# Kernel tuning notes

Hardware: AMD Instinct MI355X
Metric: run time of the kernel (lower is better)

Reference implementation:

```python
import jax, jax.numpy as jnp
import numpy as np

N = 50000      # num_nodes
E = 500000     # num_edges
D_IN = 128     # in_features
D_OUT = 128    # out_features
D_REL = 128    # nrela_dim
NEG_SLOPE = 0.2   # LeakyReLU alpha
RATIO = 0.5       # float ratio -> simple (non-schedule) branch
LN_EPS = 1e-5


def setup_inputs() -> dict:
    key = jax.random.key(0)
    ks = jax.random.split(key, 8)
    edge_index = jax.random.randint(ks[0], (2, E), 0, N, dtype=jnp.int64)
    x = jax.random.normal(ks[1], (N, D_IN), dtype=jnp.float32)
    edge_type_embed = jax.random.normal(ks[2], (E, D_REL), dtype=jnp.float32)
    # learned params (xavier-ish scale)
    W = jax.random.normal(ks[3], (4, 2 * D_OUT + D_REL, D_OUT), dtype=jnp.float32) * 0.05
    a = jax.random.normal(ks[4], (4, D_OUT, 1), dtype=jnp.float32) * 0.05
    xw = jax.random.normal(ks[5], (D_IN, D_OUT), dtype=jnp.float32) * (1.0 / np.sqrt(D_IN))
    xb = jnp.zeros((D_OUT,), dtype=jnp.float32)
    gamma = jnp.ones((D_OUT,), dtype=jnp.float32)
    beta = jnp.zeros((D_OUT,), dtype=jnp.float32)
    return {"edge_index": edge_index, "x": x, "edge_type_embed": edge_type_embed,
            "W": W, "a": a, "xw": xw, "xb": xb, "gamma": gamma, "beta": beta}


def _segment_softmax(score, seg, num_segments):
    # per-source-node softmax over edges (matches torch_geometric softmax util)
    seg_max = jax.ops.segment_max(score, seg, num_segments=num_segments)
    seg_max = jnp.where(jnp.isfinite(seg_max), seg_max, 0.0)  # empty segments
    e = jnp.exp(score - seg_max[seg])
    denom = jax.ops.segment_sum(e, seg, num_segments=num_segments)
    return e / (denom[seg] + 1e-16)


def _one_iter(edge_index, xc, ete, Wi, ai):
    src, dst = edge_index[0], edge_index[1]
    # [E, 2*D_OUT + D_REL] @ [2*D_OUT+D_REL, D_OUT] -> [E, D_OUT]
    edge_h = jnp.concatenate([xc[src], xc[dst], ete], axis=1) @ Wi
    score = jax.nn.leaky_relu(jnp.squeeze(edge_h @ ai, -1), NEG_SLOPE)  # [E]
    alpha = _segment_softmax(score, src, N)
    k = int(E * RATIO)
    _, idx = jax.lax.top_k(alpha, k)
    mask = jnp.zeros((E,), dtype=bool).at[idx].set(True)
    alpha = jnp.where(mask, alpha, 0.0)
    # scatter-add weighted messages back to source nodes
    return jax.ops.segment_sum(alpha[:, None] * edge_h, src, num_segments=N)


def reference(edge_index, x, edge_type_embed, W, a, xw, xb, gamma, beta):
    xc = x @ xw + xb  # x_linear
    for i in range(4):  # fixed 4 aggregation iterations (float-ratio branch)
        xc = _one_iter(edge_index, xc, edge_type_embed, W[i], a[i])
    xc = jax.nn.elu(xc)  # concat=True
    mu = jnp.mean(xc, axis=-1, keepdims=True)
    var = jnp.var(xc, axis=-1, keepdims=True)
    return (xc - mu) * jax.lax.rsqrt(var + LN_EPS) * gamma + beta
```

## Files before the change

kernel.cpp:

```cpp
#include <hip/hip_runtime.h>
#include <math.h>

#define DOUT 128

typedef unsigned short u16;
typedef __attribute__((ext_vector_type(8))) short bf16x8;
typedef __attribute__((ext_vector_type(4))) float f32x4;

static __device__ __forceinline__ f32x4 mfma16x16x32(bf16x8 a, bf16x8 b, f32x4 c) {
  return __builtin_amdgcn_mfma_f32_16x16x32_bf16(a, b, c, 0, 0, 0);
}

static __device__ __forceinline__ short bf16i(int v) {
  return (short)(__float_as_uint((float)v) >> 16);
}

static __device__ __forceinline__ float wsum64(float v) {
#pragma unroll
  for (int off = 32; off > 0; off >>= 1) v += __shfl_xor(v, off, 64);
  return v;
}
static __device__ __forceinline__ float wmax64(float v) {
#pragma unroll
  for (int off = 32; off > 0; off >>= 1) v = fmaxf(v, __shfl_xor(v, off, 64));
  return v;
}
static __device__ __forceinline__ float rsumg(float v) {
  v += __shfl_xor(v, 16, 64);
  v += __shfl_xor(v, 32, 64);
  return v;
}

static __device__ __forceinline__ void split3(float x, u16& h, u16& m, u16& l) {
  unsigned u = __float_as_uint(x);
  unsigned rh = u + 0x7FFFu + ((u >> 16) & 1u);
  h = (u16)(rh >> 16);
  float hf = __uint_as_float(rh & 0xFFFF0000u);
  float d1 = x - hf;
  unsigned v = __float_as_uint(d1);
  unsigned rm = v + 0x7FFFu + ((v >> 16) & 1u);
  m = (u16)(rm >> 16);
  float mf = __uint_as_float(rm & 0xFFFF0000u);
  float d2 = d1 - mf;
  unsigned w2 = __float_as_uint(d2);
  unsigned rl = w2 + 0x7FFFu + ((w2 >> 16) & 1u);
  l = (u16)(rl >> 16);
}

static __device__ __forceinline__ void split3pk(float x0, float x1,
                                                unsigned& h, unsigned& m, unsigned& l) {
  unsigned hp, mp, lp;
  asm("v_cvt_pk_bf16_f32 %0, %1, %2" : "=v"(hp) : "v"(x0), "v"(x1));
  float d0 = x0 - __uint_as_float(hp << 16);
  float d1 = x1 - __uint_as_float(hp & 0xFFFF0000u);
  asm("v_cvt_pk_bf16_f32 %0, %1, %2" : "=v"(mp) : "v"(d0), "v"(d1));
  float e0 = d0 - __uint_as_float(mp << 16);
  float e1 = d1 - __uint_as_float(mp & 0xFFFF0000u);
  asm("v_cvt_pk_bf16_f32 %0, %1, %2" : "=v"(lp) : "v"(e0), "v"(e1));
  h = hp; m = mp; l = lp;
}
static __device__ __forceinline__ void split34pk(float4 v, uint2& h, uint2& m, uint2& lo) {
  split3pk(v.x, v.y, h.x, m.x, lo.x);
  split3pk(v.z, v.w, h.y, m.y, lo.y);
}

__global__ void zero_detect_kernel(int* __restrict__ degcur, unsigned* __restrict__ hists,
                                   unsigned* __restrict__ rep, int* __restrict__ candcnt4,
                                   int N, const void* __restrict__ ei, int* __restrict__ flag,
                                   int E) {
  int i = blockIdx.x * blockDim.x + threadIdx.x;
  if (i < N) degcur[i] = 0;
  if (i < 4096) hists[i] = 0u;
  if (i < 32768) rep[i] = 0u;
  if (i < 4) candcnt4[i] = 0;
  const int* p = (const int*)ei;
  int lim = (E < 65536) ? E : 65536;
  int any = 0;
  for (int j = i; j < lim; j += gridDim.x * blockDim.x) any |= (p[2 * j + 1] != 0);
  if (__any(any))
    if ((threadIdx.x & 63) == 0 && any) atomicOr(flag, 1);
}

__global__ void cvt_deg_kernel(const void* __restrict__ ei, const int* __restrict__ flag,
                               int* __restrict__ src, int* __restrict__ dst,
                               int* __restrict__ degcur, int E) {
  int i = blockIdx.x * blockDim.x + threadIdx.x;
  if (i >= E) return;
  int s, d;
  if (*flag) { const int* p = (const int*)ei; s = p[i]; d = p[E + i]; }
  else { const long long* p = (const long long*)ei; s = (int)p[i]; d = (int)p[(size_t)E + i]; }
  src[i] = s;
  dst[i] = d;
  atomicAdd(&degcur[s], 1);
}

__global__ void scan_rowptr_kernel(int* __restrict__ degcur, int* __restrict__ rowptr, int N) {
  const int tid = threadIdx.x;
  const int lane = tid & 63, wid = tid >> 6;
  __shared__ int wsumS[16];
  __shared__ int sbase;
  if (tid == 0) sbase = 0;
  __syncthreads();
  for (int base = 0; base < N; base += 1024) {
    int i = base + tid;
    int v = (i < N) ? degcur[i] : 0;
    int x = v;
#pragma unroll
    for (int off = 1; off < 64; off <<= 1) {
      int y = __shfl_up(x, off, 64);
      if (lane >= off) x += y;
    }
    if (lane == 63) wsumS[wid] = x;
    __syncthreads();
    int wbase = 0;
#pragma unroll
    for (int w2 = 0; w2 < 16; ++w2) wbase += (w2 < wid) ? wsumS[w2] : 0;
    int excl = sbase + wbase + x - v;
    if (i < N) { rowptr[i] = excl; degcur[i] = excl; }
    __syncthreads();
    if (tid == 1023) sbase += wbase + x;
    __syncthreads();
  }
  if (tid == 0) rowptr[N] = sbase;
}

__global__ void scatter_kernel(const int* __restrict__ src, int* __restrict__ cursor,
                               int* __restrict__ eids, int E) {
  int e = blockIdx.x * blockDim.x + threadIdx.x;
  if (e >= E) return;
  int p = atomicAdd(&cursor[src[e]], 1);
  eids[p] = e;
}

__global__ void sort_eids_kernel(const int* __restrict__ rowptr, int* __restrict__ eids, int N) {
  int n = blockIdx.x * blockDim.x + threadIdx.x;
  if (n >= N) return;
  int p0 = rowptr[n], p1 = rowptr[n + 1];
  for (int i = p0 + 1; i < p1; ++i) {
    int key = eids[i];
    int j = i - 1;
    while (j >= p0 && eids[j] > key) { eids[j + 1] = eids[j]; --j; }
    eids[j + 1] = key;
  }
}

__global__ void wprep_kernel(const float* __restrict__ W, const float* __restrict__ a,
                             float* __restrict__ wa_all, const float* __restrict__ xw,
                             u16* __restrict__ wtH, u16* __restrict__ wtM,
                             u16* __restrict__ wtL) {
  int blk = blockIdx.x;
  int tid = threadIdx.x;
  if (blk < 4) {
    int it = blk, k = tid;
    const float* row = W + ((size_t)it * 384 + k) * DOUT;
    const float* ai = a + (size_t)it * DOUT;
    float acc = 0.f;
    for (int j = 0; j < DOUT; ++j) acc = fmaf(row[j], ai[j], acc);
    wa_all[it * 384 + k] = acc;
    return;
  }
  __shared__ int muS[32];
  {
    int lw = tid & 63, g = lw >> 4;
    bf16x8 aEnc;
#pragma unroll
    for (int j = 0; j < 8; ++j) aEnc[j] = bf16i(8 * g + j + 1);
    f32x4 z = {0.f, 0.f, 0.f, 0.f};
    for (int t0 = 0; t0 < 32; ++t0) {
      int g0 = t0 >> 3, j0 = t0 & 7;
      bf16x8 bOne;
#pragma unroll
      for (int j = 0; j < 8; ++j)
        bOne[j] = (g == g0 && j == j0) ? (short)0x3F80 : (short)0;
      f32x4 d = mfma16x16x32(aEnc, bOne, z);
      if (tid == t0) muS[t0] = ((int)(d[0] + 0.5f) - 1) & 31;
    }
  }
  __syncthreads();
  int b = blk - 4;
  int set, ks;
  const float* srcp;
  if (b < 4) { set = 0; ks = b; srcp = xw; }
  else { set = 1 + (b - 4) / 12; ks = (b - 4) % 12; srcp = W + (size_t)(set - 1) * 384 * DOUT; }
  size_t base = ((size_t)set * 12 + ks) * 4096;
  for (int i = tid; i < 4096; i += blockDim.x) {
    int col = i >> 5, t = i & 31;
    float x = srcp[(size_t)(ks * 32 + muS[t]) * DOUT + col];
    u16 h, m, l;
    split3(x, h, m, l);
    wtH[base + i] = h;
    wtM[base + i] = m;
    wtL[base + i] = l;
  }
}

__global__ __launch_bounds__(256) void et4_kernel(const float* __restrict__ ete,
                                                  const float* __restrict__ wa_all,
                                                  const int* __restrict__ eids,
                                                  const int* __restrict__ dst,
                                                  int* __restrict__ dstp, int* __restrict__ pos,
                                                  float* __restrict__ et4, int E) {
  __shared__ float4 w3s[4][32];
  int tid = threadIdx.x;
  if (tid < 128) {
    int it = tid >> 5, k4 = tid & 31;
    const float* base = wa_all + it * 384 + 256 + k4 * 4;
    w3s[it][k4] = make_float4(base[0], base[1], base[2], base[3]);
  }
  __syncthreads();
  int p = blockIdx.x * blockDim.x + tid;
  if (p >= E) return;
  int e = eids[p];
  dstp[p] = dst[e];
  pos[e] = p;
  const float4* row = (const float4*)(ete + (size_t)e * DOUT);
  float a0 = 0.f, a1 = 0.f, a2 = 0.f, a3 = 0.f;
#pragma unroll
  for (int k4 = 0; k4 < 32; ++k4) {
    float4 r = row[k4];
    float4 w0 = w3s[0][k4], w1 = w3s[1][k4], w2 = w3s[2][k4], w3v = w3s[3][k4];
    a0 = fmaf(r.x, w0.x, fmaf(r.y, w0.y, fmaf(r.z, w0.z, fmaf(r.w, w0.w, a0))));
    a1 = fmaf(r.x, w1.x, fmaf(r.y, w1.y, fmaf(r.z, w1.z, fmaf(r.w, w1.w, a1))));
    a2 = fmaf(r.x, w2.x, fmaf(r.y, w2.y, fmaf(r.z, w2.z, fmaf(r.w, w2.w, a2))));
    a3 = fmaf(r.x, w3v.x, fmaf(r.y, w3v.y, fmaf(r.z, w3v.z, fmaf(r.w, w3v.w, a3))));
  }
  et4[p] = a0;
  et4[(size_t)E + p] = a1;
  et4[(size_t)2 * E + p] = a2;
  et4[(size_t)3 * E + p] = a3;
}

__global__ __launch_bounds__(256) void softmax_kernel(
    const int* __restrict__ rowptr, const int* __restrict__ dstp,
    const float* __restrict__ pa, const float* __restrict__ qa, const float* __restrict__ et4,
    int it, int E, float* __restrict__ alpha, unsigned* __restrict__ rep0, int N) {
  __shared__ unsigned lh[256];
  int tid = threadIdx.x;
  lh[tid] = 0u;
  __syncthreads();
  const float* etp = et4 + (size_t)it * E;
  int w = (int)(((size_t)blockIdx.x * blockDim.x + tid) >> 6);
  int lane = tid & 63;
  if (w < N) {
    int p0 = rowptr[w], p1 = rowptr[w + 1];
    int deg = p1 - p0;
    if (deg > 0) {
      float pan = pa[w];
      if (deg <= 64) {
        int p = p0 + lane;
        int ok = (p < p1);
        float sv = -3.402823466e38f;
        if (ok) {
          float s = pan + qa[dstp[p]] + etp[p];
          sv = (s >= 0.f) ? s : 0.2f * s;
        }
        float m = wmax64(sv);
        float ee = ok ? expf(sv - m) : 0.f;
        float den = 0.f;
        for (int i = 0; i < deg; ++i) den += __shfl(ee, i, 64);
        den += 1e-16f;
        if (ok) {
          float av = ee / den;
          alpha[p] = av;
          atomicAdd(&lh[__float_as_uint(av) >> 24], 1u);
        }
      } else if (deg <= 256) {
        float sv[4]; int okv[4];
#pragma unroll
        for (int u = 0; u < 4; ++u) {
          int p = p0 + u * 64 + lane;
          if (p < p1) {
            okv[u] = 1;
            float s = pan + qa[dstp[p]] + etp[p];
            sv[u] = (s >= 0.f) ? s : 0.2f * s;
          } else { okv[u] = 0; sv[u] = -3.402823466e38f; }
        }
        float m = fmaxf(fmaxf(sv[0], sv[1]), fmaxf(sv[2], sv[3]));
        m = wmax64(m);
        float ssum = 0.f;
#pragma unroll
        for (int u = 0; u < 4; ++u)
          if (okv[u]) { sv[u] = expf(sv[u] - m); ssum += sv[u]; }
        ssum = wsum64(ssum);
        float den = ssum + 1e-16f;
#pragma unroll
        for (int u = 0; u < 4; ++u)
          if (okv[u]) {
            float av = sv[u] / den;
            alpha[p0 + u * 64 + lane] = av;
            atomicAdd(&lh[__float_as_uint(av) >> 24], 1u);
          }
      } else {
        float m = -3.402823466e38f;
        for (int p = p0 + lane; p < p1; p += 64) {
          float s = pan + qa[dstp[p]] + etp[p];
          s = (s >= 0.f) ? s : 0.2f * s;
          m = fmaxf(m, s);
        }
        m = wmax64(m);
        float ssum = 0.f;
        for (int p = p0 + lane; p < p1; p += 64) {
          float s = pan + qa[dstp[p]] + etp[p];
          s = (s >= 0.f) ? s : 0.2f * s;
          ssum += expf(s - m);
        }
        ssum = wsum64(ssum);
        float den = ssum + 1e-16f;
        for (int p = p0 + lane; p < p1; p += 64) {
          float s = pan + qa[dstp[p]] + etp[p];
          s = (s >= 0.f) ? s : 0.2f * s;
          float av = expf(s - m) / den;
          alpha[p] = av;
          atomicAdd(&lh[__float_as_uint(av) >> 24], 1u);
        }
      }
    }
  }
  __syncthreads();
  if (lh[tid]) atomicAdd(&rep0[(blockIdx.x & 31) * 256 + tid], lh[tid]);
}

__device__ __forceinline__ void scan256_one(const unsigned* __restrict__ hist, unsigned krem_in,
                                            unsigned* lds, unsigned* res,
                                            unsigned& bin, unsigned& krem_out) {
  int t = threadIdx.x;
  lds[t] = hist[t];
  __syncthreads();
  for (int off = 1; off < 256; off <<= 1) {
    unsigned add = (t + off < 256) ? lds[t + off] : 0u;
    __syncthreads();
    lds[t] += add;
    __syncthreads();
  }
  {
    unsigned above = (t == 255) ? 0u : lds[t + 1];
    if (lds[t] >= krem_in && above < krem_in) { res[0] = (unsigned)t; res[1] = krem_in - above; }
  }
  __syncthreads();
  bin = res[0];
  krem_out = res[1];
  __syncthreads();
}

__global__ __launch_bounds__(256) void hist1_kernel(const float* __restrict__ alpha,
                                                    const unsigned* __restrict__ rep0,
                                                    unsigned* __restrict__ hists_it,
                                                    unsigned* __restrict__ scanres,
                                                    unsigned Ktop, int E) {
  __shared__ unsigned lds[256], res2[2], lh[256];
  int t = threadIdx.x;
  unsigned v = 0u;
#pragma unroll
  for (int r = 0; r < 32; ++r) v += rep0[r * 256 + t];
  lds[t] = v;
  __syncthreads();
  for (int off = 1; off < 256; off <<= 1) {
    unsigned add = (t + off < 256) ? lds[t + off] : 0u;
    __syncthreads();
    lds[t] += add;
    __syncthreads();
  }
  {
    unsigned above = (t == 255) ? 0u : lds[t + 1];
    if (lds[t] >= Ktop && above < Ktop) { res2[0] = (unsigned)t; res2[1] = Ktop - above; }
  }
  __syncthreads();
  unsigned bin0 = res2[0];
  if (blockIdx.x == 0 && t == 0) { scanres[0] = bin0; scanres[1] = res2[1]; }
  lh[t] = 0u;
  __syncthreads();
  unsigned* myh = hists_it + 256;
  for (int e = blockIdx.x * blockDim.x + t; e < E; e += gridDim.x * blockDim.x) {
    unsigned b = __float_as_uint(alpha[e]);
    if ((b >> 24) == bin0) atomicAdd(&lh[(b >> 16) & 0xFFu], 1u);
  }
  __syncthreads();
  if (lh[t]) atomicAdd(&myh[t], lh[t]);
}

__global__ __launch_bounds__(256) void hist2_kernel(const float* __restrict__ alpha,
                                                    unsigned* __restrict__ hists_it,
                                                    unsigned* __restrict__ scanres, int E) {
  __shared__ unsigned lds[256], res2[2], lh[256];
  int t = threadIdx.x;
  unsigned pref8 = scanres[0], krem0 = scanres[1];
  unsigned bin1, krem1;
  scan256_one(hists_it + 256, krem0, lds, res2, bin1, krem1);
  unsigned pref16 = (pref8 << 8) | bin1;
  if (blockIdx.x == 0 && t == 0) { scanres[2] = pref16; scanres[3] = krem1; }
  lh[t] = 0u;
  __syncthreads();
  unsigned* myh = hists_it + 512;
  for (int e = blockIdx.x * blockDim.x + t; e < E; e += gridDim.x * blockDim.x) {
    unsigned b = __float_as_uint(alpha[e]);
    if ((b >> 16) == pref16) atomicAdd(&lh[(b >> 8) & 0xFFu], 1u);
  }
  __syncthreads();
  if (lh[t]) atomicAdd(&myh[t], lh[t]);
}

__global__ __launch_bounds__(256) void hist3c_kernel(const float* __restrict__ alpha,
                                                     unsigned* __restrict__ hists_it,
                                                     unsigned* __restrict__ scanres,
                                                     int* __restrict__ candList,
                                                     int* __restrict__ candCnt, int E) {
  __shared__ unsigned lds[256], res2[2], lh[256];
  int t = threadIdx.x;
  unsigned pref16 = scanres[2], krem1 = scanres[3];
  unsigned bin2, krem2;
  scan256_one(hists_it + 512, krem1, lds, res2, bin2, krem2);
  unsigned pref24 = (pref16 << 8) | bin2;
  if (blockIdx.x == 0 && t == 0) { scanres[4] = pref24; scanres[5] = krem2; }
  lh[t] = 0u;
  __syncthreads();
  unsigned* myh = hists_it + 768;
  for (int e = blockIdx.x * blockDim.x + t; e < E; e += gridDim.x * blockDim.x) {
    unsigned b = __float_as_uint(alpha[e]);
    if ((b >> 8) == pref24) {
      atomicAdd(&lh[b & 0xFFu], 1u);
      int p = atomicAdd(candCnt, 1);
      if (p < 4096) candList[p] = e;
    }
  }
  __syncthreads();
  if (lh[t]) atomicAdd(&myh[t], lh[t]);
}

__global__ __launch_bounds__(1024) void resolve24_kernel(
    const float* __restrict__ alpha, float* __restrict__ amask,
    const unsigned* __restrict__ hists_it, const unsigned* __restrict__ scanres,
    const int* __restrict__ candList, const int* __restrict__ candCnt,
    const int* __restrict__ eids, const int* __restrict__ pos,
    int* __restrict__ header, int E) {
  __shared__ unsigned lds[256], res2[2];
  int tid = threadIdx.x;
  unsigned pref24 = scanres[4], krem2 = scanres[5];
  {
    int t = tid;
    if (t < 256) lds[t] = hists_it[768 + t];
    __syncthreads();
    for (int off = 1; off < 256; off <<= 1) {
      unsigned add = 0u;
      if (t < 256 && t + off < 256) add = lds[t + off];
      __syncthreads();
      if (t < 256) lds[t] += add;
      __syncthreads();
    }
    if (t < 256) {
      unsigned above = (t == 255) ? 0u : lds[t + 1];
      if (lds[t] >= krem2 && above < krem2) { res2[0] = (unsigned)t; res2[1] = krem2 - above; }
    }
    __syncthreads();
  }
  unsigned thr = (pref24 << 8) | res2[0];
  int needT = (int)res2[1];
  __syncthreads();
  int cc = *candCnt;
  __shared__ int tiel[4096];
  __shared__ int tiec;
  if (tid == 0) tiec = 0;
  __syncthreads();
  if (cc <= 4096) {
    for (int i = tid; i < cc; i += blockDim.x) {
      int p = candList[i];
      if (__float_as_uint(alpha[p]) == thr) {
        int q = atomicAdd(&tiec, 1);
        tiel[q] = eids[p];
      }
    }
    __syncthreads();
    int ce = tiec;
    int dropc = ce - needT;
    if (dropc <= 0) {
      if (tid == 0) { header[0] = 0; header[1] = (int)thr; header[2] = 0; }
      return;
    }
    if (dropc <= 64) {
      int sortN = 64;
      while (sortN < ce) sortN <<= 1;
      for (int i = tid; i < sortN; i += blockDim.x)
        if (i >= ce) tiel[i] = 0x7fffffff;
      __syncthreads();
      for (int k = 2; k <= sortN; k <<= 1) {
        for (int j = k >> 1; j > 0; j >>= 1) {
          for (int i = tid; i < sortN; i += blockDim.x) {
            int ixj = i ^ j;
            if (ixj > i) {
              int v0 = tiel[i], v1 = tiel[ixj];
              bool up = ((i & k) == 0);
              if ((v0 > v1) == up) { tiel[i] = v1; tiel[ixj] = v0; }
            }
          }
          __syncthreads();
        }
      }
      if (tid == 0) { header[0] = 0; header[1] = (int)thr; header[2] = dropc; }
      for (int i = tid; i < dropc; i += blockDim.x) header[3 + i] = tiel[needT + i];
      return;
    }
  }
  if (tid == 0) { header[0] = 1; }
  __shared__ int wtot[16];
  __shared__ int sbase;
  if (tid == 0) sbase = 0;
  __syncthreads();
  int lane = tid & 63, wid = tid >> 6;
  for (int base = 0; base < E; base += 1024) {
    int e = base + tid;
    float a = 0.f; int f = 0; unsigned b = 0u;
    if (e < E) { a = alpha[pos[e]]; b = __float_as_uint(a); f = (b == thr) ? 1 : 0; }
    int x = f;
#pragma unroll
    for (int off = 1; off < 64; off <<= 1) {
      int y = __shfl_up(x, off, 64);
      if (lane >= off) x += y;
    }
    if (lane == 63) wtot[wid] = x;
    __syncthreads();
    int wbase = 0;
#pragma unroll
    for (int w2 = 0; w2 < 16; ++w2) wbase += (w2 < wid) ? wtot[w2] : 0;
    if (e < E) {
      float outv = 0.f;
      if (b > thr) outv = a;
      else if (f && (sbase + wbase + x - f) < needT) outv = a;
      amask[e] = outv;
    }
    __syncthreads();
    if (tid == 1023) sbase += wbase + x;
    __syncthreads();
  }
}

static __device__ __forceinline__ float edge_w2(float av, const float* __restrict__ amask,
                                                const int* __restrict__ hdr, int flg,
                                                unsigned thr, int dc, int e) {
  if (flg) return amask[e];
  unsigned b = __float_as_uint(av);
  if (b > thr) return av;
  if (b == thr) {
    for (int j = 0; j < dc; ++j)
      if (hdr[3 + j] == e) return 0.f;
    return av;
  }
  return 0.f;
}

__global__ void agg_kernel(const int* __restrict__ rowptr, const int* __restrict__ eids,
                           const int* __restrict__ dstp, const float* __restrict__ alpha,
                           const float* __restrict__ amask, const int* __restrict__ hdr,
                           const float* __restrict__ xc, const float* __restrict__ ete,
                           float* __restrict__ sa, float* __restrict__ vbuf,
                           float* __restrict__ tbuf, int N) {
  int w = (int)(((size_t)blockIdx.x * blockDim.x + threadIdx.x) >> 6);
  int lane = threadIdx.x & 63;
  if (w >= N) return;
  const int flg = hdr[0];
  const unsigned thr = (unsigned)hdr[1];
  const int dc = hdr[2];
  int p0 = rowptr[w], p1 = rowptr[w + 1];
  int deg = p1 - p0;
  const int half = lane >> 5;
  const int l32 = lane & 31;
  const float4* xc4 = (const float4*)xc;
  const float4* et4p = (const float4*)ete;
  float4 acc = make_float4(0.f, 0.f, 0.f, 0.f);
  float s = 0.f;
  if (deg <= 64) {
    int p = p0 + lane;
    int e = -1; float am = 0.f; int dd = 0;
    if (p < p1) { e = eids[p]; am = edge_w2(alpha[p], amask, hdr, flg, thr, dc, e); dd = dstp[p]; }
    for (int i = 0; i < deg; ++i) {
      float a = __shfl(am, i, 64);
      if (a != 0.f) {
        int ei = __shfl(e, i, 64);
        int di = __shfl(dd, i, 64);
        const float4* b = half ? (et4p + (size_t)ei * 32) : (xc4 + (size_t)di * 32);
        float4 r = b[l32];
        acc.x = fmaf(a, r.x, acc.x); acc.y = fmaf(a, r.y, acc.y);
        acc.z = fmaf(a, r.z, acc.z); acc.w = fmaf(a, r.w, acc.w);
        s += a;
      }
    }
  } else {
    for (int p = p0; p < p1; ++p) {
      int e0 = eids[p];
      float a0 = edge_w2(alpha[p], amask, hdr, flg, thr, dc, e0);
      if (a0 != 0.f) {
        int d0 = dstp[p];
        const float4* b0 = half ? (et4p + (size_t)e0 * 32) : (xc4 + (size_t)d0 * 32);
        float4 r = b0[l32];
        acc.x = fmaf(a0, r.x, acc.x); acc.y = fmaf(a0, r.y, acc.y);
        acc.z = fmaf(a0, r.z, acc.z); acc.w = fmaf(a0, r.w, acc.w);
        s += a0;
      }
    }
  }
  if (half == 0) ((float4*)vbuf)[(size_t)w * 32 + l32] = acc;
  else           ((float4*)tbuf)[(size_t)w * 32 + l32] = acc;
  if (lane == 0) sa[w] = s;
}

__global__ __launch_bounds__(256) void gemm_mfma_kernel(
    const float* __restrict__ A0, const float* __restrict__ A1, const float* __restrict__ A2,
    const float* __restrict__ sca, const u16* __restrict__ wtH, const u16* __restrict__ wtM,
    const u16* __restrict__ wtL, const float* __restrict__ bias, float* __restrict__ C,
    int N, int nseg,
    const float* __restrict__ wa_next, float* __restrict__ pa, float* __restrict__ qa,
    const float* __restrict__ gamma, const float* __restrict__ beta,
    float* __restrict__ outp, int epi) {
  __shared__ __align__(16) char smem[61440];
  u16 (*AsH)[40] = (u16(*)[40])(smem);
  u16 (*AsM)[40] = (u16(*)[40])(smem + 10240);
  u16 (*AsL)[40] = (u16(*)[40])(smem + 20480);
  u16 (*BsH)[40] = (u16(*)[40])(smem + 30720);
  u16 (*BsM)[40] = (u16(*)[40])(smem + 40960);
  u16 (*BsL)[40] = (u16(*)[40])(smem + 51200);
  const int tid = threadIdx.x;
  const int m0 = blockIdx.x * 128;
  const int K = DOUT * nseg;
  const int w = tid >> 6, l = tid & 63;
  const int cb = l & 15, g = l >> 4;

  int rowlab[4], collab[4];
  {
    bf16x8 enc, ones;
#pragma unroll
    for (int j = 0; j < 8; ++j) { enc[j] = bf16i(cb + 1); ones[j] = (short)0x3F80; }
    f32x4 z = {0.f, 0.f, 0.f, 0.f};
    f32x4 dR = mfma16x16x32(enc, ones, z);
    f32x4 dC = mfma16x16x32(ones, enc, z);
#pragma unroll
    for (int r = 0; r < 4; ++r) {
      rowlab[r] = ((int)(dR[r] * (1.f / 32.f) + 0.5f) - 1) & 15;
      collab[r] = ((int)(dC[r] * (1.f / 32.f) + 0.5f) - 1) & 15;
    }
  }

  f32x4 acc[2][8];
#pragma unroll
  for (int i = 0; i < 2; ++i)
#pragma unroll
    for (int j = 0; j < 8; ++j) acc[i][j] = (f32x4){0.f, 0.f, 0.f, 0.f};

  const int srow = tid >> 1, shalf = tid & 1;
  const int grow_s = m0 + srow;
  float scv = 1.f;
  if (sca && grow_s < N) scv = sca[grow_s];

  auto loadA = [&](int kc, float4& v0, float4& v1, float4& v2, float4& v3) {
    const int seg = kc >> 7;
    const float* Ap = (seg == 0) ? A0 : (seg == 1) ? A1 : A2;
    v0 = make_float4(0.f, 0.f, 0.f, 0.f); v1 = v0; v2 = v0; v3 = v0;
    if (grow_s < N) {
      const float4* p = (const float4*)(Ap + (size_t)grow_s * DOUT + (kc & 127) + shalf * 16);
      v0 = p[0]; v1 = p[1]; v2 = p[2]; v3 = p[3];
      if (seg == 0 && sca) {
        v0.x *= scv; v0.y *= scv; v0.z *= scv; v0.w *= scv;
        v1.x *= scv; v1.y *= scv; v1.z *= scv; v1.w *= scv;
        v2.x *= scv; v2.y *= scv; v2.z *= scv; v2.w *= scv;
        v3.x *= scv; v3.y *= scv; v3.z *= scv; v3.w *= scv;
      }
    }
  };
  auto loadB = [&](int kc, uint4& h0, uint4& h1, uint4& m0u, uint4& m1u, uint4& l0u,
                   uint4& l1u) {
    size_t sb = (size_t)(kc >> 5) << 12;
    const uint4* gh = (const uint4*)(wtH + sb) + tid * 2;
    const uint4* gm = (const uint4*)(wtM + sb) + tid * 2;
    const uint4* gl = (const uint4*)(wtL + sb) + tid * 2;
    h0 = gh[0]; h1 = gh[1];
    m0u = gm[0]; m1u = gm[1];
    l0u = gl[0]; l1u = gl[1];
  };

  float4 av0, av1, av2, av3, nv0, nv1, nv2, nv3;
  uint4 bh0, bh1, bm0u, bm1u, bl0u, bl1u, nh0, nh1, nm0, nm1, nl0, nl1;
  loadA(0, av0, av1, av2, av3);
  loadB(0, bh0, bh1, bm0u, bm1u, bl0u, bl1u);

  const int nks = K >> 5;
  for (int ks = 0; ks < nks; ++ks) {
    const int kc = ks << 5;
    {
      uint2 h0, m0v, l0, h1, m1v, l1, h2, m2v, l2, h3, m3v, l3;
      split34pk(av0, h0, m0v, l0); split34pk(av1, h1, m1v, l1);
      split34pk(av2, h2, m2v, l2); split34pk(av3, h3, m3v, l3);
      *(uint4*)&AsH[srow][shalf * 16]     = make_uint4(h0.x, h0.y, h1.x, h1.y);
      *(uint4*)&AsH[srow][shalf * 16 + 8] = make_uint4(h2.x, h2.y, h3.x, h3.y);
      *(uint4*)&AsM[srow][shalf * 16]     = make_uint4(m0v.x, m0v.y, m1v.x, m1v.y);
      *(uint4*)&AsM[srow][shalf * 16 + 8] = make_uint4(m2v.x, m2v.y, m3v.x, m3v.y);
      *(uint4*)&AsL[srow][shalf * 16]     = make_uint4(l0.x, l0.y, l1.x, l1.y);
      *(uint4*)&AsL[srow][shalf * 16 + 8] = make_uint4(l2.x, l2.y, l3.x, l3.y);
      *(uint4*)&BsH[srow][shalf * 16]     = bh0;
      *(uint4*)&BsH[srow][shalf * 16 + 8] = bh1;
      *(uint4*)&BsM[srow][shalf * 16]     = bm0u;
      *(uint4*)&BsM[srow][shalf * 16 + 8] = bm1u;
      *(uint4*)&BsL[srow][shalf * 16]     = bl0u;
      *(uint4*)&BsL[srow][shalf * 16 + 8] = bl1u;
    }
    if (ks + 1 < nks) {
      loadA(kc + 32, nv0, nv1, nv2, nv3);
      loadB(kc + 32, nh0, nh1, nm0, nm1, nl0, nl1);
    }
    __syncthreads();
    bf16x8 aH0 = *(const bf16x8*)&AsH[w * 32 + cb][g * 8];
    bf16x8 aH1 = *(const bf16x8*)&AsH[w * 32 + 16 + cb][g * 8];
    bf16x8 aM0 = *(const bf16x8*)&AsM[w * 32 + cb][g * 8];
    bf16x8 aM1 = *(const bf16x8*)&AsM[w * 32 + 16 + cb][g * 8];
    bf16x8 aL0 = *(const bf16x8*)&AsL[w * 32 + cb][g * 8];
    bf16x8 aL1 = *(const bf16x8*)&AsL[w * 32 + 16 + cb][g * 8];
#pragma unroll
    for (int ct = 0; ct < 8; ++ct) {
      bf16x8 bH = *(const bf16x8*)&BsH[ct * 16 + cb][g * 8];
      bf16x8 bM = *(const bf16x8*)&BsM[ct * 16 + cb][g * 8];
      bf16x8 bL = *(const bf16x8*)&BsL[ct * 16 + cb][g * 8];
      acc[0][ct] = mfma16x16x32(aH0, bH, acc[0][ct]);
      acc[1][ct] = mfma16x16x32(aH1, bH, acc[1][ct]);
      acc[0][ct] = mfma16x16x32(aM0, bH, acc[0][ct]);
      acc[1][ct] = mfma16x16x32(aM1, bH, acc[1][ct]);
      acc[0][ct] = mfma16x16x32(aL0, bH, acc[0][ct]);
      acc[1][ct] = mfma16x16x32(aL1, bH, acc[1][ct]);
      acc[0][ct] = mfma16x16x32(aH0, bM, acc[0][ct]);
      acc[1][ct] = mfma16x16x32(aH1, bM, acc[1][ct]);
      acc[0][ct] = mfma16x16x32(aM0, bM, acc[0][ct]);
      acc[1][ct] = mfma16x16x32(aM1, bM, acc[1][ct]);
      acc[0][ct] = mfma16x16x32(aH0, bL, acc[0][ct]);
      acc[1][ct] = mfma16x16x32(aH1, bL, acc[1][ct]);
    }
    __syncthreads();
    av0 = nv0; av1 = nv1; av2 = nv2; av3 = nv3;
    bh0 = nh0; bh1 = nh1; bm0u = nm0; bm1u = nm1; bl0u = nl0; bl1u = nl1;
  }

  float* slab = (float*)(smem + (size_t)w * 8448);
  const int row16 = l & 15;
  const int csel = (l >> 4) * 32;
#pragma unroll
  for (int rt = 0; rt < 2; ++rt) {
#pragma unroll
    for (int ct = 0; ct < 8; ++ct)
#pragma unroll
      for (int r = 0; r < 4; ++r)
        slab[rowlab[r] * 132 + ct * 16 + collab[r]] = acc[rt][ct][r];
    __syncthreads();
    int grow = m0 + w * 32 + rt * 16 + row16;
    float v[32];
#pragma unroll
    for (int q = 0; q < 8; ++q) {
      float4 t4 = *(float4*)&slab[row16 * 132 + csel + q * 4];
      v[q * 4 + 0] = t4.x; v[q * 4 + 1] = t4.y; v[q * 4 + 2] = t4.z; v[q * 4 + 3] = t4.w;
    }
    if (bias) {
#pragma unroll
      for (int q = 0; q < 8; ++q) {
        float4 bb = *(const float4*)(bias + csel + q * 4);
        v[q * 4 + 0] += bb.x; v[q * 4 + 1] += bb.y; v[q * 4 + 2] += bb.z; v[q * 4 + 3] += bb.w;
      }
    }
    if (epi == 2) {
#pragma unroll
      for (int i = 0; i < 32; ++i) v[i] = (v[i] > 0.f) ? v[i] : expm1f(v[i]);
      float s = 0.f;
#pragma unroll
      for (int i = 0; i < 32; ++i) s += v[i];
      s = rsumg(s);
      float mu = s * (1.f / 128.f);
      float sq = 0.f;
#pragma unroll
      for (int i = 0; i < 32; ++i) { float d = v[i] - mu; sq += d * d; }
      sq = rsumg(sq);
      float rstd = rsqrtf(sq * (1.f / 128.f) + 1e-5f);
      if (grow < N) {
#pragma unroll
        for (int q = 0; q < 8; ++q) {
          float4 ga = *(const float4*)(gamma + csel + q * 4);
          float4 be = *(const float4*)(beta + csel + q * 4);
          float4 o;
          o.x = (v[q * 4 + 0] - mu) * rstd * ga.x + be.x;
          o.y = (v[q * 4 + 1] - mu) * rstd * ga.y + be.y;
          o.z = (v[q * 4 + 2] - mu) * rstd * ga.z + be.z;
          o.w = (v[q * 4 + 3] - mu) * rstd * ga.w + be.w;
          *(float4*)(outp + (size_t)grow * DOUT + csel + q * 4) = o;
        }
      }
    } else {
      if (grow < N) {
#pragma unroll
        for (int q = 0; q < 8; ++q)
          *(float4*)(C + (size_t)grow * DOUT + csel + q * 4) =
              make_float4(v[q * 4 + 0], v[q * 4 + 1], v[q * 4 + 2], v[q * 4 + 3]);
      }
      if (epi == 1) {
        float pp = 0.f, qq = 0.f;
#pragma unroll
        for (int i = 0; i < 32; ++i) {
          pp = fmaf(v[i], wa_next[csel + i], pp);
          qq = fmaf(v[i], wa_next[128 + csel + i], qq);
        }
        pp = rsumg(pp);
        qq = rsumg(qq);
        if ((l >> 4) == 0 && grow < N) { pa[grow] = pp; qa[grow] = qq; }
      }
    }
    __syncthreads();
  }
}

extern "C" void kernel_launch(void* const* d_in, const int* in_sizes, int n_in,
                              void* d_out, int out_size, void* d_ws, size_t ws_size,
                              hipStream_t stream) {
  const int E = in_sizes[0] / 2;
  const int N = in_sizes[1] / DOUT;
  const unsigned Ktop = (unsigned)(E / 2);

  const void*  ei    = d_in[0];
  const float* x     = (const float*)d_in[1];
  const float* ete   = (const float*)d_in[2];
  const float* W     = (const float*)d_in[3];
  const float* a     = (const float*)d_in[4];
  const float* xw    = (const float*)d_in[5];
  const float* xb    = (const float*)d_in[6];
  const float* gamma = (const float*)d_in[7];
  const float* beta  = (const float*)d_in[8];
  float* out = (float*)d_out;

  size_t off = 0;
  auto take = [&](size_t bytes) -> char* {
    char* p = (char*)d_ws + off;
    off += (bytes + 255) & ~(size_t)255;
    return p;
  };
  int*      src32   = (int*)take((size_t)E * 4);
  int*      dst32   = (int*)take((size_t)E * 4);
  int*      rowptr  = (int*)take(((size_t)N + 1) * 4);
  int*      degcur  = (int*)take((size_t)N * 4);
  int*      eids    = (int*)take((size_t)E * 4);
  int*      dstp    = (int*)take((size_t)E * 4);
  int*      pos     = (int*)take((size_t)E * 4);
  float*    pa      = (float*)take((size_t)N * 4);
  float*    qa      = (float*)take((size_t)N * 4);
  float*    wa_all  = (float*)take(4 * 384 * 4);
  float*    alpha   = (float*)take((size_t)E * 4);
  float*    amask   = (float*)take((size_t)E * 4);
  float*    sa      = (float*)take((size_t)N * 4);
  float*    vbuf    = (float*)take((size_t)N * DOUT * 4);
  float*    tbuf    = (float*)take((size_t)N * DOUT * 4);
  float*    xcA     = (float*)take((size_t)N * DOUT * 4);
  float*    xcB     = (float*)take((size_t)N * DOUT * 4);
  float*    et4     = (float*)take((size_t)E * 4 * 4);
  unsigned* hists   = (unsigned*)take(4 * 4 * 256 * 4);
  unsigned* rep     = (unsigned*)take(4 * 32 * 256 * 4);
  int*      candcnt4= (int*)take(64);
  int*      flag    = (int*)take(64);
  int*      candList= (int*)take(4096 * 4);
  int*      header  = (int*)take(4 * 80 * 4);
  u16*      wtH     = (u16*)take((size_t)5 * 12 * 4096 * 2);
  u16*      wtM     = (u16*)take((size_t)5 * 12 * 4096 * 2);
  u16*      wtL     = (u16*)take((size_t)5 * 12 * 4096 * 2);
  unsigned* scanres = (unsigned*)take(4 * 8 * 4);
  (void)ws_size; (void)n_in; (void)out_size;

  const int TB  = 256;
  const int gE  = (E + TB - 1) / TB;
  const int gN  = (N + TB - 1) / TB;
  const int gN4 = (N + 3) / 4;
  const int gM  = (N + 127) / 128;

  (void)hipMemsetAsync(flag, 0, 4, stream);
  zero_detect_kernel<<<gN, TB, 0, stream>>>(degcur, hists, rep, candcnt4, N, ei, flag, E);
  cvt_deg_kernel<<<gE, TB, 0, stream>>>(ei, flag, src32, dst32, degcur, E);
  scan_rowptr_kernel<<<1, 1024, 0, stream>>>(degcur, rowptr, N);
  scatter_kernel<<<gE, TB, 0, stream>>>(src32, degcur, eids, E);
  sort_eids_kernel<<<gN, TB, 0, stream>>>(rowptr, eids, N);
  wprep_kernel<<<56, 384, 0, stream>>>(W, a, wa_all, xw, wtH, wtM, wtL);
  et4_kernel<<<gE, TB, 0, stream>>>(ete, wa_all, eids, dst32, dstp, pos, et4, E);
  gemm_mfma_kernel<<<gM, 256, 0, stream>>>(x, nullptr, nullptr, nullptr, wtH, wtM, wtL, xb,
                                           xcA, N, 1, wa_all, pa, qa, nullptr, nullptr,
                                           nullptr, 1);

  float* bufs[2] = {xcA, xcB};
  for (int it = 0; it < 4; ++it) {
    const float* xc = bufs[it & 1];
    float* xn = bufs[(it & 1) ^ 1];
    unsigned* hists_it = hists + it * 1024;
    unsigned* rep_it = rep + it * 8192;
    unsigned* sres_it = scanres + it * 8;
    int* hdr_it = header + it * 80;
    const u16* wH = wtH + (size_t)(it + 1) * 12 * 4096;
    const u16* wM = wtM + (size_t)(it + 1) * 12 * 4096;
    const u16* wL = wtL + (size_t)(it + 1) * 12 * 4096;

    softmax_kernel<<<gN4, TB, 0, stream>>>(rowptr, dstp, pa, qa, et4, it, E, alpha,
                                           rep_it, N);
    hist1_kernel<<<384, 256, 0, stream>>>(alpha, rep_it, hists_it, sres_it, Ktop, E);
    hist2_kernel<<<384, 256, 0, stream>>>(alpha, hists_it, sres_it, E);
    hist3c_kernel<<<384, 256, 0, stream>>>(alpha, hists_it, sres_it, candList,
                                           candcnt4 + it, E);
    resolve24_kernel<<<1, 1024, 0, stream>>>(alpha, amask, hists_it, sres_it, candList,
                                             candcnt4 + it, eids, pos, hdr_it, E);
    agg_kernel<<<gN4, TB, 0, stream>>>(rowptr, eids, dstp, alpha, amask, hdr_it,
                                       xc, ete, sa, vbuf, tbuf, N);
    if (it < 3)
      gemm_mfma_kernel<<<gM, 256, 0, stream>>>(xc, vbuf, tbuf, sa, wH, wM, wL, nullptr, xn,
                                               N, 3, wa_all + (it + 1) * 384, pa, qa,
                                               nullptr, nullptr, nullptr, 1);
    else
      gemm_mfma_kernel<<<gM, 256, 0, stream>>>(xc, vbuf, tbuf, sa, wH, wM, wL, nullptr, xn,
                                               N, 3, nullptr, pa, qa, gamma, beta, out, 2);
  }
}
```

Measured before the change: 825.3 us.

## Compact radix-select candidates into lists and fold third histogram pass into resolver

```diff
diff --git a/kernel.cpp b/kernel.cpp
--- a/kernel.cpp
+++ b/kernel.cpp
@@ -2,6 +2,8 @@
 #include <math.h>
 
 #define DOUT 128
+#define C8CAP 262144
+#define C16CAP 32768
 
 typedef unsigned short u16;
 typedef __attribute__((ext_vector_type(8))) short bf16x8;
@@ -29,6 +31,21 @@
   v += __shfl_xor(v, 16, 64);
   v += __shfl_xor(v, 32, 64);
   return v;
+}
+
+static __device__ __forceinline__ void wappend(int match, int val, int* cnt,
+                                               int* list, int cap) {
+  unsigned long long mk = __ballot(match);
+  if (mk == 0ull) return;
+  int lane = threadIdx.x & 63;
+  int ldr = __ffsll((unsigned long long)mk) - 1;
+  int base = 0;
+  if (lane == ldr) base = atomicAdd(cnt, (int)__popcll(mk));
+  base = __shfl(base, ldr, 64);
+  if (match) {
+    int slot = base + (int)__popcll(mk & ((1ull << lane) - 1ull));
+    if (slot < cap) list[slot] = val;
+  }
 }
 
 static __device__ __forceinline__ void split3(float x, u16& h, u16& m, u16& l) {
@@ -65,14 +82,14 @@
 }
 
 __global__ void zero_detect_kernel(int* __restrict__ degcur, unsigned* __restrict__ hists,
-                                   unsigned* __restrict__ rep, int* __restrict__ candcnt4,
+                                   unsigned* __restrict__ rep, int* __restrict__ cnts,
                                    int N, const void* __restrict__ ei, int* __restrict__ flag,
                                    int E) {
   int i = blockIdx.x * blockDim.x + threadIdx.x;
   if (i < N) degcur[i] = 0;
   if (i < 4096) hists[i] = 0u;
   if (i < 32768) rep[i] = 0u;
-  if (i < 4) candcnt4[i] = 0;
+  if (i < 8) cnts[i] = 0;
   const int* p = (const int*)ei;
   int lim = (E < 65536) ? E : 65536;
   int any = 0;
@@ -320,34 +337,14 @@
   if (lh[tid]) atomicAdd(&rep0[(blockIdx.x & 31) * 256 + tid], lh[tid]);
 }
 
-__device__ __forceinline__ void scan256_one(const unsigned* __restrict__ hist, unsigned krem_in,
-                                            unsigned* lds, unsigned* res,
-                                            unsigned& bin, unsigned& krem_out) {
-  int t = threadIdx.x;
-  lds[t] = hist[t];
-  __syncthreads();
-  for (int off = 1; off < 256; off <<= 1) {
-    unsigned add = (t + off < 256) ? lds[t + off] : 0u;
-    __syncthreads();
-    lds[t] += add;
-    __syncthreads();
-  }
-  {
-    unsigned above = (t == 255) ? 0u : lds[t + 1];
-    if (lds[t] >= krem_in && above < krem_in) { res[0] = (unsigned)t; res[1] = krem_in - above; }
-  }
-  __syncthreads();
-  bin = res[0];
-  krem_out = res[1];
-  __syncthreads();
-}
-
 __global__ __launch_bounds__(256) void hist1_kernel(const float* __restrict__ alpha,
                                                     const unsigned* __restrict__ rep0,
                                                     unsigned* __restrict__ hists_it,
                                                     unsigned* __restrict__ scanres,
+                                                    int* __restrict__ cand8,
+                                                    int* __restrict__ cnt8,
                                                     unsigned Ktop, int E) {
-  __shared__ unsigned lds[256], res2[2], lh[256];
+  __shared__ unsigned lds[256], res2[3], lh[256];
   int t = threadIdx.x;
   unsigned v = 0u;
 #pragma unroll
@@ -362,17 +359,24 @@
   }
   {
     unsigned above = (t == 255) ? 0u : lds[t + 1];
-    if (lds[t] >= Ktop && above < Ktop) { res2[0] = (unsigned)t; res2[1] = Ktop - above; }
-  }
-  __syncthreads();
-  unsigned bin0 = res2[0];
-  if (blockIdx.x == 0 && t == 0) { scanres[0] = bin0; scanres[1] = res2[1]; }
+    if (lds[t] >= Ktop && above < Ktop) {
+      res2[0] = (unsigned)t; res2[1] = Ktop - above; res2[2] = lds[t] - above;
+    }
+  }
+  __syncthreads();
+  unsigned bin0 = res2[0], cnt0 = res2[2];
+  if (blockIdx.x == 0 && t == 0) {
+    scanres[0] = bin0; scanres[1] = res2[1]; scanres[6] = cnt0;
+  }
+  int collect = (cnt0 <= (unsigned)C8CAP);
   lh[t] = 0u;
   __syncthreads();
   unsigned* myh = hists_it + 256;
   for (int e = blockIdx.x * blockDim.x + t; e < E; e += gridDim.x * blockDim.x) {
     unsigned b = __float_as_uint(alpha[e]);
-    if ((b >> 24) == bin0) atomicAdd(&lh[(b >> 16) & 0xFFu], 1u);
+    int match = ((b >> 24) == bin0);
+    if (match) atomicAdd(&lh[(b >> 16) & 0xFFu], 1u);
+    if (collect) wappend(match, e, cnt8, cand8, C8CAP);
   }
   __syncthreads();
   if (lh[t]) atomicAdd(&myh[t], lh[t]);
@@ -380,123 +384,162 @@
 
 __global__ __launch_bounds__(256) void hist2_kernel(const float* __restrict__ alpha,
                                                     unsigned* __restrict__ hists_it,
-                                                    unsigned* __restrict__ scanres, int E) {
-  __shared__ unsigned lds[256], res2[2], lh[256];
+                                                    unsigned* __restrict__ scanres,
+                                                    const int* __restrict__ cand8,
+                                                    int* __restrict__ cand16,
+                                                    int* __restrict__ cnt16, int E) {
+  __shared__ unsigned lds[256], res2[3], lh[256];
   int t = threadIdx.x;
-  unsigned pref8 = scanres[0], krem0 = scanres[1];
-  unsigned bin1, krem1;
-  scan256_one(hists_it + 256, krem0, lds, res2, bin1, krem1);
+  unsigned pref8 = scanres[0], krem0 = scanres[1], cnt0 = scanres[6];
+  lds[t] = hists_it[256 + t];
+  __syncthreads();
+  for (int off = 1; off < 256; off <<= 1) {
+    unsigned add = (t + off < 256) ? lds[t + off] : 0u;
+    __syncthreads();
+    lds[t] += add;
+    __syncthreads();
+  }
+  {
+    unsigned above = (t == 255) ? 0u : lds[t + 1];
+    if (lds[t] >= krem0 && above < krem0) {
+      res2[0] = (unsigned)t; res2[1] = krem0 - above; res2[2] = lds[t] - above;
+    }
+  }
+  __syncthreads();
+  unsigned bin1 = res2[0], krem1 = res2[1], cnt1 = res2[2];
   unsigned pref16 = (pref8 << 8) | bin1;
-  if (blockIdx.x == 0 && t == 0) { scanres[2] = pref16; scanres[3] = krem1; }
+  if (blockIdx.x == 0 && t == 0) {
+    scanres[2] = pref16; scanres[3] = krem1; scanres[7] = cnt1;
+  }
+  int collect = (cnt1 <= (unsigned)C16CAP);
   lh[t] = 0u;
   __syncthreads();
   unsigned* myh = hists_it + 512;
-  for (int e = blockIdx.x * blockDim.x + t; e < E; e += gridDim.x * blockDim.x) {
-    unsigned b = __float_as_uint(alpha[e]);
-    if ((b >> 16) == pref16) atomicAdd(&lh[(b >> 8) & 0xFFu], 1u);
+  const int stride = gridDim.x * blockDim.x;
+  if (cnt0 <= (unsigned)C8CAP) {
+    for (int i = blockIdx.x * blockDim.x + t; i < (int)cnt0; i += stride) {
+      int p = cand8[i];
+      unsigned b = __float_as_uint(alpha[p]);
+      int match = ((b >> 16) == pref16);
+      if (match) atomicAdd(&lh[(b >> 8) & 0xFFu], 1u);
+      if (collect) wappend(match, p, cnt16, cand16, C16CAP);
+    }
+  } else {
+    for (int e = blockIdx.x * blockDim.x + t; e < E; e += stride) {
+      unsigned b = __float_as_uint(alpha[e]);
+      int match = ((b >> 16) == pref16);
+      if (match) atomicAdd(&lh[(b >> 8) & 0xFFu], 1u);
+      if (collect) wappend(match, e, cnt16, cand16, C16CAP);
+    }
   }
   __syncthreads();
   if (lh[t]) atomicAdd(&myh[t], lh[t]);
 }
 
-__global__ __launch_bounds__(256) void hist3c_kernel(const float* __restrict__ alpha,
-                                                     unsigned* __restrict__ hists_it,
-                                                     unsigned* __restrict__ scanres,
-                                                     int* __restrict__ candList,
-                                                     int* __restrict__ candCnt, int E) {
-  __shared__ unsigned lds[256], res2[2], lh[256];
-  int t = threadIdx.x;
-  unsigned pref16 = scanres[2], krem1 = scanres[3];
-  unsigned bin2, krem2;
-  scan256_one(hists_it + 512, krem1, lds, res2, bin2, krem2);
-  unsigned pref24 = (pref16 << 8) | bin2;
-  if (blockIdx.x == 0 && t == 0) { scanres[4] = pref24; scanres[5] = krem2; }
-  lh[t] = 0u;
-  __syncthreads();
-  unsigned* myh = hists_it + 768;
-  for (int e = blockIdx.x * blockDim.x + t; e < E; e += gridDim.x * blockDim.x) {
-    unsigned b = __float_as_uint(alpha[e]);
-    if ((b >> 8) == pref24) {
-      atomicAdd(&lh[b & 0xFFu], 1u);
-      int p = atomicAdd(candCnt, 1);
-      if (p < 4096) candList[p] = e;
-    }
-  }
-  __syncthreads();
-  if (lh[t]) atomicAdd(&myh[t], lh[t]);
-}
-
-__global__ __launch_bounds__(1024) void resolve24_kernel(
+__global__ __launch_bounds__(1024) void resolve3_kernel(
     const float* __restrict__ alpha, float* __restrict__ amask,
     const unsigned* __restrict__ hists_it, const unsigned* __restrict__ scanres,
-    const int* __restrict__ candList, const int* __restrict__ candCnt,
-    const int* __restrict__ eids, const int* __restrict__ pos,
+    const int* __restrict__ cand16, const int* __restrict__ eids, const int* __restrict__ pos,
     int* __restrict__ header, int E) {
-  __shared__ unsigned lds[256], res2[2];
+  __shared__ unsigned lds[256], res2[2], lh[256];
   int tid = threadIdx.x;
-  unsigned pref24 = scanres[4], krem2 = scanres[5];
+  unsigned pref16 = scanres[2], krem1 = scanres[3], cnt1 = scanres[7];
   {
-    int t = tid;
-    if (t < 256) lds[t] = hists_it[768 + t];
+    if (tid < 256) lds[tid] = hists_it[512 + tid];
     __syncthreads();
     for (int off = 1; off < 256; off <<= 1) {
       unsigned add = 0u;
-      if (t < 256 && t + off < 256) add = lds[t + off];
+      if (tid < 256 && tid + off < 256) add = lds[tid + off];
       __syncthreads();
-      if (t < 256) lds[t] += add;
+      if (tid < 256) lds[tid] += add;
       __syncthreads();
     }
-    if (t < 256) {
-      unsigned above = (t == 255) ? 0u : lds[t + 1];
-      if (lds[t] >= krem2 && above < krem2) { res2[0] = (unsigned)t; res2[1] = krem2 - above; }
+    if (tid < 256) {
+      unsigned above = (tid == 255) ? 0u : lds[tid + 1];
+      if (lds[tid] >= krem1 && above < krem1) { res2[0] = (unsigned)tid; res2[1] = krem1 - above; }
+    }
+    __syncthreads();
+  }
+  unsigned pref24 = (pref16 << 8) | res2[0];
+  unsigned krem2 = res2[1];
+  __syncthreads();
+  const int haveList = (cnt1 <= (unsigned)C16CAP);
+  if (tid < 256) lh[tid] = 0u;
+  __syncthreads();
+  if (haveList) {
+    for (int i = tid; i < (int)cnt1; i += 1024) {
+      unsigned b = __float_as_uint(alpha[cand16[i]]);
+      if ((b >> 8) == pref24) atomicAdd(&lh[b & 0xFFu], 1u);
+    }
+  } else {
+    for (int e = tid; e < E; e += 1024) {
+      unsigned b = __float_as_uint(alpha[e]);
+      if ((b >> 8) == pref24) atomicAdd(&lh[b & 0xFFu], 1u);
+    }
+  }
+  __syncthreads();
+  {
+    if (tid < 256) lds[tid] = lh[tid];
+    __syncthreads();
+    for (int off = 1; off < 256; off <<= 1) {
+      unsigned add = 0u;
+      if (tid < 256 && tid + off < 256) add = lds[tid + off];
+      __syncthreads();
+      if (tid < 256) lds[tid] += add;
+      __syncthreads();
+    }
+    if (tid < 256) {
+      unsigned above = (tid == 255) ? 0u : lds[tid + 1];
+      if (lds[tid] >= krem2 && above < krem2) { res2[0] = (unsigned)tid; res2[1] = krem2 - above; }
     }
     __syncthreads();
   }
   unsigned thr = (pref24 << 8) | res2[0];
   int needT = (int)res2[1];
   __syncthreads();
-  int cc = *candCnt;
   __shared__ int tiel[4096];
   __shared__ int tiec;
   if (tid == 0) tiec = 0;
   __syncthreads();
-  if (cc <= 4096) {
-    for (int i = tid; i < cc; i += blockDim.x) {
-      int p = candList[i];
+  if (haveList) {
+    for (int i = tid; i < (int)cnt1; i += 1024) {
+      int p = cand16[i];
       if (__float_as_uint(alpha[p]) == thr) {
         int q = atomicAdd(&tiec, 1);
-        tiel[q] = eids[p];
+        if (q < 4096) tiel[q] = eids[p];
       }
     }
     __syncthreads();
     int ce = tiec;
-    int dropc = ce - needT;
-    if (dropc <= 0) {
-      if (tid == 0) { header[0] = 0; header[1] = (int)thr; header[2] = 0; }
-      return;
-    }
-    if (dropc <= 64) {
-      int sortN = 64;
-      while (sortN < ce) sortN <<= 1;
-      for (int i = tid; i < sortN; i += blockDim.x)
-        if (i >= ce) tiel[i] = 0x7fffffff;
-      __syncthreads();
-      for (int k = 2; k <= sortN; k <<= 1) {
-        for (int j = k >> 1; j > 0; j >>= 1) {
-          for (int i = tid; i < sortN; i += blockDim.x) {
-            int ixj = i ^ j;
-            if (ixj > i) {
-              int v0 = tiel[i], v1 = tiel[ixj];
-              bool up = ((i & k) == 0);
-              if ((v0 > v1) == up) { tiel[i] = v1; tiel[ixj] = v0; }
+    if (ce <= 4096) {
+      int dropc = ce - needT;
+      if (dropc <= 0) {
+        if (tid == 0) { header[0] = 0; header[1] = (int)thr; header[2] = 0; }
+        return;
+      }
+      if (dropc <= 64) {
+        int sortN = 64;
+        while (sortN < ce) sortN <<= 1;
+        for (int i = tid; i < sortN; i += blockDim.x)
+          if (i >= ce) tiel[i] = 0x7fffffff;
+        __syncthreads();
+        for (int k = 2; k <= sortN; k <<= 1) {
+          for (int j = k >> 1; j > 0; j >>= 1) {
+            for (int i = tid; i < sortN; i += blockDim.x) {
+              int ixj = i ^ j;
+              if (ixj > i) {
+                int v0 = tiel[i], v1 = tiel[ixj];
+                bool up = ((i & k) == 0);
+                if ((v0 > v1) == up) { tiel[i] = v1; tiel[ixj] = v0; }
+              }
             }
+            __syncthreads();
           }
-          __syncthreads();
         }
-      }
-      if (tid == 0) { header[0] = 0; header[1] = (int)thr; header[2] = dropc; }
-      for (int i = tid; i < dropc; i += blockDim.x) header[3 + i] = tiel[needT + i];
-      return;
+        if (tid == 0) { header[0] = 0; header[1] = (int)thr; header[2] = dropc; }
+        for (int i = tid; i < dropc; i += blockDim.x) header[3 + i] = tiel[needT + i];
+        return;
+      }
     }
   }
   if (tid == 0) { header[0] = 1; }
@@ -851,9 +894,10 @@
   float*    et4     = (float*)take((size_t)E * 4 * 4);
   unsigned* hists   = (unsigned*)take(4 * 4 * 256 * 4);
   unsigned* rep     = (unsigned*)take(4 * 32 * 256 * 4);
-  int*      candcnt4= (int*)take(64);
+  int*      cnts    = (int*)take(64);
   int*      flag    = (int*)take(64);
-  int*      candList= (int*)take(4096 * 4);
+  int*      cand8   = (int*)take((size_t)C8CAP * 4);
+  int*      cand16  = (int*)take((size_t)C16CAP * 4);
   int*      header  = (int*)take(4 * 80 * 4);
   u16*      wtH     = (u16*)take((size_t)5 * 12 * 4096 * 2);
   u16*      wtM     = (u16*)take((size_t)5 * 12 * 4096 * 2);
@@ -868,7 +912,7 @@
   const int gM  = (N + 127) / 128;
 
   (void)hipMemsetAsync(flag, 0, 4, stream);
-  zero_detect_kernel<<<gN, TB, 0, stream>>>(degcur, hists, rep, candcnt4, N, ei, flag, E);
+  zero_detect_kernel<<<gN, TB, 0, stream>>>(degcur, hists, rep, cnts, N, ei, flag, E);
   cvt_deg_kernel<<<gE, TB, 0, stream>>>(ei, flag, src32, dst32, degcur, E);
   scan_rowptr_kernel<<<1, 1024, 0, stream>>>(degcur, rowptr, N);
   scatter_kernel<<<gE, TB, 0, stream>>>(src32, degcur, eids, E);
@@ -893,12 +937,12 @@
 
     softmax_kernel<<<gN4, TB, 0, stream>>>(rowptr, dstp, pa, qa, et4, it, E, alpha,
                                            rep_it, N);
-    hist1_kernel<<<384, 256, 0, stream>>>(alpha, rep_it, hists_it, sres_it, Ktop, E);
-    hist2_kernel<<<384, 256, 0, stream>>>(alpha, hists_it, sres_it, E);
-    hist3c_kernel<<<384, 256, 0, stream>>>(alpha, hists_it, sres_it, candList,
-                                           candcnt4 + it, E);
-    resolve24_kernel<<<1, 1024, 0, stream>>>(alpha, amask, hists_it, sres_it, candList,
-                                             candcnt4 + it, eids, pos, hdr_it, E);
+    hist1_kernel<<<384, 256, 0, stream>>>(alpha, rep_it, hists_it, sres_it, cand8,
+                                          cnts + it * 2, Ktop, E);
+    hist2_kernel<<<384, 256, 0, stream>>>(alpha, hists_it, sres_it, cand8, cand16,
+                                          cnts + it * 2 + 1, E);
+    resolve3_kernel<<<1, 1024, 0, stream>>>(alpha, amask, hists_it, sres_it, cand16,
+                                            eids, pos, hdr_it, E);
     agg_kernel<<<gN4, TB, 0, stream>>>(rowptr, eids, dstp, alpha, amask, hdr_it,
                                        xc, ete, sa, vbuf, tbuf, N);
     if (it < 3)
```

Result: slower. 931.8 us (+12.9%).
